# Optimization experiments

Measured on AMD Instinct MI355X. Metric: run time of the kernel, lower is better.

## Reference

```python
import jax, jax.numpy as jnp
import numpy as np

N_NODES = 50000
N_EDGES = 800000
D_IN = 128
D_OUT = 128


def setup_inputs() -> dict:
    key = jax.random.key(0)
    k1, k2, k3, k4, k5 = jax.random.split(key, 5)
    x = jax.random.normal(k1, (N_NODES, D_IN), dtype=jnp.float32)
    edge_index = jax.random.randint(k2, (2, N_EDGES), 0, N_NODES, dtype=jnp.int64)
    scale = 1.0 / np.sqrt(D_IN)
    W_rel = jax.random.normal(k3, (D_OUT, D_IN), dtype=jnp.float32) * scale
    b_rel = jax.random.normal(k4, (D_OUT,), dtype=jnp.float32) * scale
    W_root = jax.random.normal(k5, (D_OUT, D_IN), dtype=jnp.float32) * scale
    return {"x": x, "edge_index": edge_index, "W_rel": W_rel, "b_rel": b_rel, "W_root": W_root}


def reference(x, edge_index, W_rel, b_rel, W_root):
    # PyG GraphConv (aggr='add'):
    #   out_i = W_rel @ (sum_{j->i} x_j) + b_rel + W_root @ x_i
    # followed by ReLU (normalization=None, dropout=0 -> identity).
    src = edge_index[0]  # message source j
    dst = edge_index[1]  # message target i
    n = x.shape[0]
    agg = jax.ops.segment_sum(x[src], dst, num_segments=n)  # [N, D_IN]
    out = agg @ W_rel.T + b_rel + x @ W_root.T              # [N, D_OUT]
    return jax.nn.relu(out)
```

## Files before the change

### kernel.cpp

```cpp
#include <hip/hip_runtime.h>
#include <hip/hip_bf16.h>


#define N_NODES 50000
#define N_EDGES 800000
#define D 128
#define SLOTS 48
#define NPB 32
#define KC 32
#define SROW 136

#define CVT_N  (N_NODES * (D / 2))
#define PACK_N (8 * 8 * 64 * 8)

typedef __attribute__((ext_vector_type(8))) short short8;
typedef __attribute__((ext_vector_type(4))) float floatx4;

__device__ __forceinline__ float bf2f(unsigned short u) {
    return __uint_as_float((unsigned int)u << 16);
}
__device__ __forceinline__ unsigned short f2bf(float f) {
    __hip_bfloat16 h = __float2bfloat16(f);
    return *(unsigned short*)&h;
}

__device__ __forceinline__ int wave_detect_i64(const int* __restrict__ ei) {
    int lane = threadIdx.x & 63;
    int v = ei[2 * lane + 1];
    return __ballot(v == 0) == ~0ull;
}

__global__ __launch_bounds__(256) void zero_f4_kernel(float4* __restrict__ p, int n4) {
    int i = blockIdx.x * 256 + threadIdx.x;
    if (i < n4) p[i] = make_float4(0.f, 0.f, 0.f, 0.f);
}

__global__ void detect_kernel(const int* __restrict__ ei, int* __restrict__ flag) {
    if (threadIdx.x == 0 && blockIdx.x == 0) {
        int any = 0;
        for (int i = 0; i < 64; ++i) any |= ei[2 * i + 1];
        flag[0] = (any == 0) ? 1 : 0;
    }
}

__global__ __launch_bounds__(256) void prep_kernel(const float2* __restrict__ x2,
                                                   ushort2* __restrict__ xb2,
                                                   const float* __restrict__ Wrel,
                                                   const float* __restrict__ Wroot,
                                                   unsigned short* __restrict__ pwc,
                                                   int* __restrict__ cnt) {
    int i = blockIdx.x * 256 + threadIdx.x;
    if (i < CVT_N) {
        float2 f = x2[i];
        xb2[i] = make_ushort2(f2bf(f.x), f2bf(f.y));
    } else if (i < CVT_N + PACK_N) {
        int idx  = i - CVT_N;
        int j    = idx & 7;
        int lane = (idx >> 3) & 63;
        int n0   = (idx >> 9) & 7;
        int t    = idx >> 12;
        int n = n0 * 16 + (lane & 15);
        int k = t * 32 + (lane >> 4) * 8 + j;
        float w = (k < D) ? Wrel[n * D + k] : Wroot[n * D + (k - D)];
        pwc[idx] = f2bf(w);
    } else if (i < CVT_N + PACK_N + N_NODES + 4) {
        cnt[i - CVT_N - PACK_N] = 0;
    }
}

__global__ __launch_bounds__(256) void append_kernel(const int* __restrict__ ei,
                                                     int* __restrict__ cnt,
                                                     int* __restrict__ slots,
                                                     int* __restrict__ ovf_cnt,
                                                     int* __restrict__ ovf) {
    int i64 = wave_detect_i64(ei);
    int base = (blockIdx.x * 256 + threadIdx.x) * 4;
    if (base >= N_EDGES) return;
    int s0, s1, s2, s3, d0, d1, d2, d3;
    if (i64) {
        int4 a = *(const int4*)&ei[2 * base];
        int4 b = *(const int4*)&ei[2 * base + 4];
        s0 = a.x; s1 = a.z; s2 = b.x; s3 = b.z;
        int4 c = *(const int4*)&ei[2 * N_EDGES + 2 * base];
        int4 e = *(const int4*)&ei[2 * N_EDGES + 2 * base + 4];
        d0 = c.x; d1 = c.z; d2 = e.x; d3 = e.z;
    } else {
        int4 sv = *(const int4*)&ei[base];
        int4 dv = *(const int4*)&ei[N_EDGES + base];
        s0 = sv.x; s1 = sv.y; s2 = sv.z; s3 = sv.w;
        d0 = dv.x; d1 = dv.y; d2 = dv.z; d3 = dv.w;
    }
    bool v0 = (unsigned)s0 < N_NODES && (unsigned)d0 < N_NODES;
    bool v1 = (unsigned)s1 < N_NODES && (unsigned)d1 < N_NODES;
    bool v2 = (unsigned)s2 < N_NODES && (unsigned)d2 < N_NODES;
    bool v3 = (unsigned)s3 < N_NODES && (unsigned)d3 < N_NODES;
    int p0 = v0 ? atomicAdd(&cnt[d0], 1) : 0;
    int p1 = v1 ? atomicAdd(&cnt[d1], 1) : 0;
    int p2 = v2 ? atomicAdd(&cnt[d2], 1) : 0;
    int p3 = v3 ? atomicAdd(&cnt[d3], 1) : 0;
    if (v0) { if (p0 < SLOTS) slots[d0 * SLOTS + p0] = s0;
              else { int o = atomicAdd(ovf_cnt, 1); ovf[2 * o] = d0; ovf[2 * o + 1] = s0; } }
    if (v1) { if (p1 < SLOTS) slots[d1 * SLOTS + p1] = s1;
              else { int o = atomicAdd(ovf_cnt, 1); ovf[2 * o] = d1; ovf[2 * o + 1] = s1; } }
    if (v2) { if (p2 < SLOTS) slots[d2 * SLOTS + p2] = s2;
              else { int o = atomicAdd(ovf_cnt, 1); ovf[2 * o] = d2; ovf[2 * o + 1] = s2; } }
    if (v3) { if (p3 < SLOTS) slots[d3 * SLOTS + p3] = s3;
              else { int o = atomicAdd(ovf_cnt, 1); ovf[2 * o] = d3; ovf[2 * o + 1] = s3; } }
}

__global__ __launch_bounds__(256) void GraphConvLayer_55783035240593_kernel(
        const ushort2* __restrict__ xb2,
        const unsigned short* __restrict__ xb,
        const int* __restrict__ cnt,
        const int* __restrict__ slots,
        const int* __restrict__ ovf_cnt,
        const int* __restrict__ ovf,
        const unsigned short* __restrict__ pwc,
        const float* __restrict__ b_rel,
        float* __restrict__ out) {
    __shared__ unsigned short sA[16 * SROW];
    int wid  = threadIdx.x >> 6;
    int lane = threadIdx.x & 63;
    int node0 = blockIdx.x * 16;
    int tov = ovf_cnt[0];

    for (int li = 0; li < 4; ++li) {
        int node = node0 + wid * 4 + li;
        int kk = cnt[node];
        if (kk > SLOTS) kk = SLOTS;
        int myidx = (lane < kk) ? slots[node * SLOTS + lane] : 0;
        float ax = 0.f, ay = 0.f;
        for (int j = 0; j < kk; j += 8) {
            int s0 = __shfl(myidx, j);
            int s1 = __shfl(myidx, j + 1);
            int s2 = __shfl(myidx, j + 2);
            int s3 = __shfl(myidx, j + 3);
            int s4 = __shfl(myidx, j + 4);
            int s5 = __shfl(myidx, j + 5);
            int s6 = __shfl(myidx, j + 6);
            int s7 = __shfl(myidx, j + 7);
            ushort2 u0 = xb2[(size_t)s0 * (D / 2) + lane];
            ushort2 u1 = xb2[(size_t)s1 * (D / 2) + lane];
            ushort2 u2 = xb2[(size_t)s2 * (D / 2) + lane];
            ushort2 u3 = xb2[(size_t)s3 * (D / 2) + lane];
            ushort2 u4 = xb2[(size_t)s4 * (D / 2) + lane];
            ushort2 u5 = xb2[(size_t)s5 * (D / 2) + lane];
            ushort2 u6 = xb2[(size_t)s6 * (D / 2) + lane];
            ushort2 u7 = xb2[(size_t)s7 * (D / 2) + lane];
            float m1 = (j + 1 < kk) ? 1.f : 0.f;
            float m2 = (j + 2 < kk) ? 1.f : 0.f;
            float m3 = (j + 3 < kk) ? 1.f : 0.f;
            float m4 = (j + 4 < kk) ? 1.f : 0.f;
            float m5 = (j + 5 < kk) ? 1.f : 0.f;
            float m6 = (j + 6 < kk) ? 1.f : 0.f;
            float m7 = (j + 7 < kk) ? 1.f : 0.f;
            ax += bf2f(u0.x) + m1 * bf2f(u1.x) + m2 * bf2f(u2.x) + m3 * bf2f(u3.x)
                + m4 * bf2f(u4.x) + m5 * bf2f(u5.x) + m6 * bf2f(u6.x) + m7 * bf2f(u7.x);
            ay += bf2f(u0.y) + m1 * bf2f(u1.y) + m2 * bf2f(u2.y) + m3 * bf2f(u3.y)
                + m4 * bf2f(u4.y) + m5 * bf2f(u5.y) + m6 * bf2f(u6.y) + m7 * bf2f(u7.y);
        }
        if (tov > 0) {
            for (int t2 = 0; t2 < tov; ++t2) {
                if (ovf[2 * t2] == node) {
                    ushort2 u = xb2[(size_t)ovf[2 * t2 + 1] * (D / 2) + lane];
                    ax += bf2f(u.x);
                    ay += bf2f(u.y);
                }
            }
        }
        *(ushort2*)&sA[(wid * 4 + li) * SROW + 2 * lane] =
            make_ushort2(f2bf(ax), f2bf(ay));
    }
    __syncthreads();

    int m = lane & 15, quad = lane >> 4;
    const unsigned short* arow = &sA[m * SROW + quad * 8];
    const unsigned short* xrow = xb + (size_t)(node0 + m) * D + quad * 8;

    floatx4 acc0 = (floatx4){0.f, 0.f, 0.f, 0.f};
    floatx4 acc1 = (floatx4){0.f, 0.f, 0.f, 0.f};
#pragma unroll
    for (int t = 0; t < 8; ++t) {
        short8 afrag = (t < 4) ? *(const short8*)(arow + t * 32)
                               : *(const short8*)(xrow + (t - 4) * 32);
        const unsigned short* bb = pwc + ((size_t)(t * 8 + wid * 2) * 64 + lane) * 8;
        short8 b0 = *(const short8*)bb;
        short8 b1 = *(const short8*)(bb + 64 * 8);
        acc0 = __builtin_amdgcn_mfma_f32_16x16x32_bf16(afrag, b0, acc0, 0, 0, 0);
        acc1 = __builtin_amdgcn_mfma_f32_16x16x32_bf16(afrag, b1, acc1, 0, 0, 0);
    }

#pragma unroll
    for (int q = 0; q < 2; ++q) {
        floatx4 a = q ? acc1 : acc0;
        int n = (wid * 2 + q) * 16 + m;
        float bias = b_rel[n];
#pragma unroll
        for (int r = 0; r < 4; ++r) {
            int node = node0 + quad * 4 + r;
            out[(size_t)node * D + n] = fmaxf(a[r] + bias, 0.f);
        }
    }
}

__global__ __launch_bounds__(256) void pack_w_kernel(const float* __restrict__ W,
                                                     float* __restrict__ pw) {
    int idx = blockIdx.x * 256 + threadIdx.x;
    if (idx >= D * D) return;
    int o = idx >> 7, k = idx & 127;
    pw[k * D + o] = W[o * D + k];
}

__global__ __launch_bounds__(256) void hist_kernel(const int* __restrict__ ei,
                                                   int* __restrict__ deg) {
    int i64 = wave_detect_i64(ei);
    int base = (blockIdx.x * 256 + threadIdx.x) * 4;
    if (base >= N_EDGES) return;
    int d0, d1, d2, d3;
    if (i64) {
        int4 a = *(const int4*)&ei[2 * N_EDGES + 2 * base];
        int4 b = *(const int4*)&ei[2 * N_EDGES + 2 * base + 4];
        d0 = a.x; d1 = a.z; d2 = b.x; d3 = b.z;
    } else {
        int4 v = *(const int4*)&ei[N_EDGES + base];
        d0 = v.x; d1 = v.y; d2 = v.z; d3 = v.w;
    }
    if ((unsigned)d0 < N_NODES) atomicAdd(&deg[d0], 1);
    if ((unsigned)d1 < N_NODES) atomicAdd(&deg[d1], 1);
    if ((unsigned)d2 < N_NODES) atomicAdd(&deg[d2], 1);
    if ((unsigned)d3 < N_NODES) atomicAdd(&deg[d3], 1);
}

__device__ __forceinline__ int wave_iscan(int v, int lane) {
#pragma unroll
    for (int off = 1; off < 64; off <<= 1) {
        int u = __shfl_up(v, off, 64);
        if (lane >= off) v += u;
    }
    return v;
}

__global__ __launch_bounds__(1024) void scan_kernel(const int* __restrict__ deg,
                                                    int* __restrict__ offsets,
                                                    int* __restrict__ cursor) {
    __shared__ int wsum[16];
    __shared__ int base_s;
    int t = threadIdx.x, lane = t & 63, w = t >> 6;
    if (t == 0) { base_s = 0; offsets[0] = 0; }
    __syncthreads();
    for (int c0 = 0; c0 < N_NODES; c0 += 1024) {
        int idx = c0 + t;
        int v = (idx < N_NODES) ? deg[idx] : 0;
        int inc = wave_iscan(v, lane);
        if (lane == 63) wsum[w] = inc;
        __syncthreads();
        if (w == 0) {
            int s = (lane < 16) ? wsum[lane] : 0;
            int si = wave_iscan(s, lane);
            if (lane < 16) wsum[lane] = si - s;
        }
        __syncthreads();
        int tot = base_s + wsum[w] + inc;
        if (idx < N_NODES) {
            offsets[idx + 1] = tot;
            cursor[idx] = tot - v;
        }
        __syncthreads();
        if (t == 1023) base_s = tot;
        __syncthreads();
    }
}

__global__ __launch_bounds__(256) void reorder_kernel(const int* __restrict__ ei,
                                                      int* __restrict__ cursor,
                                                      int* __restrict__ csr_src) {
    int i64 = wave_detect_i64(ei);
    int base = (blockIdx.x * 256 + threadIdx.x) * 4;
    if (base >= N_EDGES) return;
    int s0, s1, s2, s3, d0, d1, d2, d3;
    if (i64) {
        int4 a = *(const int4*)&ei[2 * base];
        int4 b = *(const int4*)&ei[2 * base + 4];
        s0 = a.x; s1 = a.z; s2 = b.x; s3 = b.z;
        int4 c = *(const int4*)&ei[2 * N_EDGES + 2 * base];
        int4 e = *(const int4*)&ei[2 * N_EDGES + 2 * base + 4];
        d0 = c.x; d1 = c.z; d2 = e.x; d3 = e.z;
    } else {
        int4 sv = *(const int4*)&ei[base];
        int4 dv = *(const int4*)&ei[N_EDGES + base];
        s0 = sv.x; s1 = sv.y; s2 = sv.z; s3 = sv.w;
        d0 = dv.x; d1 = dv.y; d2 = dv.z; d3 = dv.w;
    }
    bool v0 = (unsigned)s0 < N_NODES && (unsigned)d0 < N_NODES;
    bool v1 = (unsigned)s1 < N_NODES && (unsigned)d1 < N_NODES;
    bool v2 = (unsigned)s2 < N_NODES && (unsigned)d2 < N_NODES;
    bool v3 = (unsigned)s3 < N_NODES && (unsigned)d3 < N_NODES;
    int p0 = v0 ? atomicAdd(&cursor[d0], 1) : 0;
    int p1 = v1 ? atomicAdd(&cursor[d1], 1) : 0;
    int p2 = v2 ? atomicAdd(&cursor[d2], 1) : 0;
    int p3 = v3 ? atomicAdd(&cursor[d3], 1) : 0;
    if (v0) csr_src[p0] = s0;
    if (v1) csr_src[p1] = s1;
    if (v2) csr_src[p2] = s2;
    if (v3) csr_src[p3] = s3;
}

__global__ __launch_bounds__(256) void gather_kernel(const float2* __restrict__ x2,
                                                     const int* __restrict__ csr_src,
                                                     const int* __restrict__ offsets,
                                                     float2* __restrict__ agg2) {
    int node = blockIdx.x * 4 + (threadIdx.x >> 6);
    int lane = threadIdx.x & 63;
    if (node >= N_NODES) return;
    int beg = offsets[node], end = offsets[node + 1];
    float2 acc = make_float2(0.f, 0.f);
    for (int e = beg; e < end; ++e) {
        int s = csr_src[e];
        float2 f = x2[(size_t)s * (D / 2) + lane];
        acc.x += f.x;
        acc.y += f.y;
    }
    agg2[(size_t)node * (D / 2) + lane] = acc;
}

__global__ __launch_bounds__(256) void scatter_kernel(const float2* __restrict__ x2,
                                                      const int* __restrict__ ei,
                                                      const int* __restrict__ flag,
                                                      float* __restrict__ agg) {
    int wave = threadIdx.x >> 6;
    int lane = threadIdx.x & 63;
    int e = blockIdx.x * 4 + wave;
    if (e >= N_EDGES) return;
    int i64 = flag ? flag[0] : 0;
    int s, d;
    if (i64) { s = ei[2 * e]; d = ei[2 * N_EDGES + 2 * e]; }
    else     { s = ei[e];     d = ei[N_EDGES + e]; }
    if ((unsigned)s >= N_NODES || (unsigned)d >= N_NODES) return;
    float2 f = x2[(size_t)s * (D / 2) + lane];
    atomicAdd(&agg[(size_t)d * D + 2 * lane + 0], f.x);
    atomicAdd(&agg[(size_t)d * D + 2 * lane + 1], f.y);
}

__global__ __launch_bounds__(256) void gemm_f32_kernel(
        const float2* __restrict__ x2,
        const float* __restrict__ pwrel,
        const float* __restrict__ pwroot,
        const float* __restrict__ b_rel,
        float* __restrict__ out) {
    __shared__ float sWrel[KC * D];
    __shared__ float sWroot[KC * D];
    __shared__ float2 sAm[NPB * (KC / 2)];
    __shared__ float2 sXm[NPB * (KC / 2)];

    int t = threadIdx.x;
    int node0 = blockIdx.x * NPB;
    int tn = t >> 5;
    int to = t & 31;

    float acc[4][4];
#pragma unroll
    for (int a = 0; a < 4; ++a)
#pragma unroll
        for (int b = 0; b < 4; ++b) acc[a][b] = 0.0f;

    for (int c = 0; c < 4; ++c) {
        __syncthreads();
#pragma unroll
        for (int r = 0; r < 4; ++r) {
            int i = r * 256 + t;
            ((float4*)sWrel)[i]  = ((const float4*)(pwrel  + c * KC * D))[i];
            ((float4*)sWroot)[i] = ((const float4*)(pwroot + c * KC * D))[i];
        }
#pragma unroll
        for (int r = 0; r < 2; ++r) {
            int i = r * 256 + t;
            int n = i >> 4, k2 = i & 15;
            int node = node0 + n;
            float2 av = make_float2(0.f, 0.f), xv = make_float2(0.f, 0.f);
            if (node < N_NODES) {
                av = ((const float2*)out)[(size_t)node * (D / 2) + c * (KC / 2) + k2];
                xv = x2[(size_t)node * (D / 2) + c * (KC / 2) + k2];
            }
            sAm[i] = av;
            sXm[i] = xv;
        }
        __syncthreads();

#pragma unroll
        for (int k2 = 0; k2 < KC / 2; ++k2) {
            float4 wr0 = *(const float4*)&sWrel[(2 * k2 + 0) * D + to * 4];
            float4 wr1 = *(const float4*)&sWrel[(2 * k2 + 1) * D + to * 4];
            float4 wt0 = *(const float4*)&sWroot[(2 * k2 + 0) * D + to * 4];
            float4 wt1 = *(const float4*)&sWroot[(2 * k2 + 1) * D + to * 4];
#pragma unroll
            for (int ni = 0; ni < 4; ++ni) {
                float2 a  = sAm[(tn * 4 + ni) * (KC / 2) + k2];
                float2 xx = sXm[(tn * 4 + ni) * (KC / 2) + k2];
                acc[ni][0] += a.x * wr0.x + a.y * wr1.x + xx.x * wt0.x + xx.y * wt1.x;
                acc[ni][1] += a.x * wr0.y + a.y * wr1.y + xx.x * wt0.y + xx.y * wt1.y;
                acc[ni][2] += a.x * wr0.z + a.y * wr1.z + xx.x * wt0.z + xx.y * wt1.z;
                acc[ni][3] += a.x * wr0.w + a.y * wr1.w + xx.x * wt0.w + xx.y * wt1.w;
            }
        }
    }

    int o0 = to * 4;
    float4 bias = *(const float4*)&b_rel[o0];
#pragma unroll
    for (int ni = 0; ni < 4; ++ni) {
        int node = node0 + tn * 4 + ni;
        if (node >= N_NODES) continue;
        float4 v;
        v.x = fmaxf(acc[ni][0] + bias.x, 0.f);
        v.y = fmaxf(acc[ni][1] + bias.y, 0.f);
        v.z = fmaxf(acc[ni][2] + bias.z, 0.f);
        v.w = fmaxf(acc[ni][3] + bias.w, 0.f);
        *(float4*)&out[(size_t)node * D + o0] = v;
    }
}

__global__ __launch_bounds__(128) void gemm_fallback_kernel(const float* __restrict__ x,
                                                            const float* __restrict__ Wrel,
                                                            const float* __restrict__ Wroot,
                                                            const float* __restrict__ b_rel,
                                                            float* __restrict__ out) {
    __shared__ float rowA[D];
    __shared__ float rowX[D];
    int node = blockIdx.x;
    int o = threadIdx.x;
    rowA[o] = out[(size_t)node * D + o];
    rowX[o] = x[(size_t)node * D + o];
    __syncthreads();
    float acc = b_rel[o];
    const float4* wr = (const float4*)&Wrel[o * D];
    const float4* wt = (const float4*)&Wroot[o * D];
#pragma unroll 8
    for (int k4 = 0; k4 < D / 4; ++k4) {
        float4 w = wr[k4], u = wt[k4];
        const float* a = &rowA[k4 * 4];
        const float* xx = &rowX[k4 * 4];
        acc += a[0] * w.x + a[1] * w.y + a[2] * w.z + a[3] * w.w
             + xx[0] * u.x + xx[1] * u.y + xx[2] * u.z + xx[3] * u.w;
    }
    __syncthreads();
    out[(size_t)node * D + o] = fmaxf(acc, 0.f);
}

extern "C" void kernel_launch(void* const* d_in, const int* in_sizes, int n_in,
                              void* d_out, int out_size, void* d_ws, size_t ws_size,
                              hipStream_t stream) {
    const float* x      = (const float*)d_in[0];
    const int*   ei     = (const int*)d_in[1];
    const float* W_rel  = (const float*)d_in[2];
    const float* b_rel  = (const float*)d_in[3];
    const float* W_root = (const float*)d_in[4];
    float*       out    = (float*)d_out;

    char* p = (char*)d_ws;
    size_t o0 = 16;
    int*            flag    = (int*)p;
    unsigned short* pwc     = (unsigned short*)(p + o0);  o0 += (size_t)PACK_N * 2;
    unsigned short* xb      = (unsigned short*)(p + o0);  o0 += (size_t)N_NODES * D * 2;
    int*            cnt     = (int*)(p + o0);             o0 += (size_t)N_NODES * 4;
    int*            ovf_cnt = (int*)(p + o0);             o0 += 16;
    int*            slots   = (int*)(p + o0);             o0 += (size_t)N_NODES * SLOTS * 4;
    int*            ovf     = (int*)(p + o0);             o0 += (size_t)N_EDGES * 8;
    const size_t need_full = o0;

    size_t m0 = 16;
    float* m_pwrel  = (float*)(p + m0);  m0 += (size_t)D * D * 4;
    float* m_pwroot = (float*)(p + m0);  m0 += (size_t)D * D * 4;
    int*   m_deg    = (int*)(p + m0);    m0 += (size_t)N_NODES * 4;
    int*   m_offs   = (int*)(p + m0);    m0 += ((size_t)N_NODES + 1) * 4 + 12;
    m0 &= ~15ull;
    int*   m_csr    = (int*)(p + m0);    m0 += (size_t)N_EDGES * 4;
    const size_t need_mid = m0;
    const size_t need_pw  = 16 + 2 * (size_t)D * D * 4;

    const int eb4 = (N_EDGES / 4 + 255) / 256;

    if (ws_size >= need_full) {
        const int prep_total = CVT_N + PACK_N + N_NODES + 4;
        prep_kernel<<<(prep_total + 255) / 256, 256, 0, stream>>>(
            (const float2*)x, (ushort2*)xb, W_rel, W_root, pwc, cnt);
        append_kernel<<<eb4, 256, 0, stream>>>(ei, cnt, slots, ovf_cnt, ovf);
        GraphConvLayer_55783035240593_kernel<<<N_NODES / 16, 256, 0, stream>>>(
            (const ushort2*)xb, xb, cnt, slots, ovf_cnt, ovf, pwc, b_rel, out);
    } else if (ws_size >= need_mid) {
        pack_w_kernel<<<64, 256, 0, stream>>>(W_rel, m_pwrel);
        pack_w_kernel<<<64, 256, 0, stream>>>(W_root, m_pwroot);
        zero_f4_kernel<<<(N_NODES / 4 + 255) / 256, 256, 0, stream>>>((float4*)m_deg,
                                                                      N_NODES / 4);
        hist_kernel<<<eb4, 256, 0, stream>>>(ei, m_deg);
        scan_kernel<<<1, 1024, 0, stream>>>(m_deg, m_offs, m_deg);
        reorder_kernel<<<eb4, 256, 0, stream>>>(ei, m_deg, m_csr);
        gather_kernel<<<N_NODES / 4, 256, 0, stream>>>((const float2*)x, m_csr,
                                                       m_offs, (float2*)out);
        gemm_f32_kernel<<<(N_NODES + NPB - 1) / NPB, 256, 0, stream>>>(
            (const float2*)x, m_pwrel, m_pwroot, b_rel, out);
    } else {
        bool have_flag = ws_size >= 16;
        bool have_pw   = ws_size >= need_pw;
        if (have_flag) detect_kernel<<<1, 64, 0, stream>>>(ei, flag);
        if (have_pw) {
            pack_w_kernel<<<64, 256, 0, stream>>>(W_rel, m_pwrel);
            pack_w_kernel<<<64, 256, 0, stream>>>(W_root, m_pwroot);
        }
        int n4 = N_NODES * D / 4;
        zero_f4_kernel<<<(n4 + 255) / 256, 256, 0, stream>>>((float4*)out, n4);
        scatter_kernel<<<N_EDGES / 4, 256, 0, stream>>>((const float2*)x, ei,
                                                        have_flag ? flag : nullptr, out);
        if (have_pw)
            gemm_f32_kernel<<<(N_NODES + NPB - 1) / NPB, 256, 0, stream>>>(
                (const float2*)x, m_pwrel, m_pwroot, b_rel, out);
        else
            gemm_fallback_kernel<<<N_NODES, 128, 0, stream>>>(x, W_rel, W_root, b_rel, out);
    }
}
```

Baseline: 172.3 us.

## Pad per-node counters to separate cache lines, halve edges per thread, shrink slots

The per-destination counters are spread with a stride of 8 ints, so the atomics for different nodes fall in different 32-byte sectors, which is meant to reduce atomic contention on shared lines. Each append thread now handles 2 edges instead of 4, giving twice as many threads for more parallelism. Slots per node drop from 48 to 40, which shrinks the slot array. The overflow counter now lives right after the padded counter array. The zeroing pass has 8x more counter memory to clear, and more edges now go down the overflow path.

```diff
diff --git a/kernel.cpp b/kernel.cpp
--- a/kernel.cpp
+++ b/kernel.cpp
@@ -5,13 +5,15 @@
 #define N_NODES 50000
 #define N_EDGES 800000
 #define D 128
-#define SLOTS 48
+#define SLOTS 40
+#define CSTR 8
 #define NPB 32
 #define KC 32
 #define SROW 136
 
 #define CVT_N  (N_NODES * (D / 2))
 #define PACK_N (8 * 8 * 64 * 8)
+#define CNT_N  (N_NODES * CSTR + 4)
 
 typedef __attribute__((ext_vector_type(8))) short short8;
 typedef __attribute__((ext_vector_type(4))) float floatx4;
@@ -63,7 +65,7 @@
         int k = t * 32 + (lane >> 4) * 8 + j;
         float w = (k < D) ? Wrel[n * D + k] : Wroot[n * D + (k - D)];
         pwc[idx] = f2bf(w);
-    } else if (i < CVT_N + PACK_N + N_NODES + 4) {
+    } else if (i < CVT_N + PACK_N + CNT_N) {
         cnt[i - CVT_N - PACK_N] = 0;
     }
 }
@@ -74,38 +76,28 @@
                                                      int* __restrict__ ovf_cnt,
                                                      int* __restrict__ ovf) {
     int i64 = wave_detect_i64(ei);
-    int base = (blockIdx.x * 256 + threadIdx.x) * 4;
+    int base = (blockIdx.x * 256 + threadIdx.x) * 2;
     if (base >= N_EDGES) return;
-    int s0, s1, s2, s3, d0, d1, d2, d3;
+    int s0, s1, d0, d1;
     if (i64) {
         int4 a = *(const int4*)&ei[2 * base];
-        int4 b = *(const int4*)&ei[2 * base + 4];
-        s0 = a.x; s1 = a.z; s2 = b.x; s3 = b.z;
+        s0 = a.x; s1 = a.z;
         int4 c = *(const int4*)&ei[2 * N_EDGES + 2 * base];
-        int4 e = *(const int4*)&ei[2 * N_EDGES + 2 * base + 4];
-        d0 = c.x; d1 = c.z; d2 = e.x; d3 = e.z;
+        d0 = c.x; d1 = c.z;
     } else {
-        int4 sv = *(const int4*)&ei[base];
-        int4 dv = *(const int4*)&ei[N_EDGES + base];
-        s0 = sv.x; s1 = sv.y; s2 = sv.z; s3 = sv.w;
-        d0 = dv.x; d1 = dv.y; d2 = dv.z; d3 = dv.w;
+        int2 sv = *(const int2*)&ei[base];
+        int2 dv = *(const int2*)&ei[N_EDGES + base];
+        s0 = sv.x; s1 = sv.y;
+        d0 = dv.x; d1 = dv.y;
     }
     bool v0 = (unsigned)s0 < N_NODES && (unsigned)d0 < N_NODES;
     bool v1 = (unsigned)s1 < N_NODES && (unsigned)d1 < N_NODES;
-    bool v2 = (unsigned)s2 < N_NODES && (unsigned)d2 < N_NODES;
-    bool v3 = (unsigned)s3 < N_NODES && (unsigned)d3 < N_NODES;
-    int p0 = v0 ? atomicAdd(&cnt[d0], 1) : 0;
-    int p1 = v1 ? atomicAdd(&cnt[d1], 1) : 0;
-    int p2 = v2 ? atomicAdd(&cnt[d2], 1) : 0;
-    int p3 = v3 ? atomicAdd(&cnt[d3], 1) : 0;
+    int p0 = v0 ? atomicAdd(&cnt[d0 * CSTR], 1) : 0;
+    int p1 = v1 ? atomicAdd(&cnt[d1 * CSTR], 1) : 0;
     if (v0) { if (p0 < SLOTS) slots[d0 * SLOTS + p0] = s0;
               else { int o = atomicAdd(ovf_cnt, 1); ovf[2 * o] = d0; ovf[2 * o + 1] = s0; } }
     if (v1) { if (p1 < SLOTS) slots[d1 * SLOTS + p1] = s1;
               else { int o = atomicAdd(ovf_cnt, 1); ovf[2 * o] = d1; ovf[2 * o + 1] = s1; } }
-    if (v2) { if (p2 < SLOTS) slots[d2 * SLOTS + p2] = s2;
-              else { int o = atomicAdd(ovf_cnt, 1); ovf[2 * o] = d2; ovf[2 * o + 1] = s2; } }
-    if (v3) { if (p3 < SLOTS) slots[d3 * SLOTS + p3] = s3;
-              else { int o = atomicAdd(ovf_cnt, 1); ovf[2 * o] = d3; ovf[2 * o + 1] = s3; } }
 }
 
 __global__ __launch_bounds__(256) void GraphConvLayer_55783035240593_kernel(
@@ -126,7 +118,7 @@
 
     for (int li = 0; li < 4; ++li) {
         int node = node0 + wid * 4 + li;
-        int kk = cnt[node];
+        int kk = cnt[node * CSTR];
         if (kk > SLOTS) kk = SLOTS;
         int myidx = (lane < kk) ? slots[node * SLOTS + lane] : 0;
         float ax = 0.f, ay = 0.f;
@@ -461,7 +453,7 @@
     int*            flag    = (int*)p;
     unsigned short* pwc     = (unsigned short*)(p + o0);  o0 += (size_t)PACK_N * 2;
     unsigned short* xb      = (unsigned short*)(p + o0);  o0 += (size_t)N_NODES * D * 2;
-    int*            cnt     = (int*)(p + o0);             o0 += (size_t)N_NODES * 4;
+    int*            cnt     = (int*)(p + o0);             o0 += (size_t)N_NODES * CSTR * 4;
     int*            ovf_cnt = (int*)(p + o0);             o0 += 16;
     int*            slots   = (int*)(p + o0);             o0 += (size_t)N_NODES * SLOTS * 4;
     int*            ovf     = (int*)(p + o0);             o0 += (size_t)N_EDGES * 8;
@@ -478,14 +470,18 @@
     const size_t need_pw  = 16 + 2 * (size_t)D * D * 4;
 
     const int eb4 = (N_EDGES / 4 + 255) / 256;
+    const int eb2 = (N_EDGES / 2 + 255) / 256;
 
     if (ws_size >= need_full) {
-        const int prep_total = CVT_N + PACK_N + N_NODES + 4;
+        const int prep_total = CVT_N + PACK_N + CNT_N;
         prep_kernel<<<(prep_total + 255) / 256, 256, 0, stream>>>(
             (const float2*)x, (ushort2*)xb, W_rel, W_root, pwc, cnt);
-        append_kernel<<<eb4, 256, 0, stream>>>(ei, cnt, slots, ovf_cnt, ovf);
+        append_kernel<<<eb2, 256, 0, stream>>>(ei, cnt, slots,
+                                               cnt + N_NODES * CSTR, ovf);
         GraphConvLayer_55783035240593_kernel<<<N_NODES / 16, 256, 0, stream>>>(
-            (const ushort2*)xb, xb, cnt, slots, ovf_cnt, ovf, pwc, b_rel, out);
+            (const ushort2*)xb, xb, cnt, slots, cnt + N_NODES * CSTR, ovf,
+            pwc, b_rel, out);
+        (void)ovf_cnt;
     } else if (ws_size >= need_mid) {
         pack_w_kernel<<<64, 256, 0, stream>>>(W_rel, m_pwrel);
         pack_w_kernel<<<64, 256, 0, stream>>>(W_root, m_pwroot);
```

Result: slower. 177.2 us (+2.9%).
